# Optimization experiments

Hardware: AMD Instinct MI355X
Metric: run time of the kernel (lower is better)

The kernel has to match this reference:

```python
import jax, jax.numpy as jnp
import numpy as np
import math

N = 100000   # nodes
E = 500000   # edges
IN_C = 128
EDGE_D = 64
HEADS = 4
OUT_C = 32
HC = HEADS * OUT_C  # 128


def setup_inputs() -> dict:
    key = jax.random.key(0)
    ks = jax.random.split(key, 12)
    s_in = 1.0 / math.sqrt(IN_C)
    s_e = 1.0 / math.sqrt(EDGE_D)
    return {
        "x": jax.random.normal(ks[0], (N, IN_C), jnp.float32),
        "edge_index": jax.random.randint(ks[1], (2, E), 0, N, dtype=jnp.int32),
        "edge_attr": jax.random.normal(ks[2], (E, EDGE_D), jnp.float32),
        "Wq": jax.random.uniform(ks[3], (HC, IN_C), jnp.float32, -s_in, s_in),
        "bq": jax.random.uniform(ks[4], (HC,), jnp.float32, -s_in, s_in),
        "Wk": jax.random.uniform(ks[5], (HC, IN_C), jnp.float32, -s_in, s_in),
        "bk": jax.random.uniform(ks[6], (HC,), jnp.float32, -s_in, s_in),
        "Wv": jax.random.uniform(ks[7], (HC, IN_C), jnp.float32, -s_in, s_in),
        "bv": jax.random.uniform(ks[8], (HC,), jnp.float32, -s_in, s_in),
        "We": jax.random.uniform(ks[9], (HC, EDGE_D), jnp.float32, -s_e, s_e),
        "Ws": jax.random.uniform(ks[10], (HC, IN_C), jnp.float32, -s_in, s_in),
        "bs": jax.random.uniform(ks[11], (HC,), jnp.float32, -s_in, s_in),
    }


def reference(x, edge_index, edge_attr, Wq, bq, Wk, bk, Wv, bv, We, Ws, bs):
    src = edge_index[0]
    dst = edge_index[1]
    x_i = x[dst]                       # [E, IN_C] target-node feats
    x_j = x[src]                       # [E, IN_C] source-node feats

    e = (edge_attr @ We.T).reshape(E, HEADS, OUT_C)
    q = (x_i @ Wq.T + bq).reshape(E, HEADS, OUT_C)
    k = (x_j @ Wk.T + bk).reshape(E, HEADS, OUT_C) + e

    alpha = jnp.sum(q * k, axis=-1) / jnp.sqrt(jnp.float32(OUT_C))  # [E, H]
    # Faithful to the source: GLOBAL per-column max (not per-segment), then
    # segment-sum of exponentials over destination nodes.
    m = jnp.max(alpha, axis=0)                                      # [H]
    exp_a = jnp.exp(alpha - m)                                      # [E, H]
    denom = jax.ops.segment_sum(exp_a, dst, num_segments=N)         # [N, H]
    alpha = exp_a / (denom[dst] + 1e-16)                            # [E, H]

    v = (x_j @ Wv.T + bv).reshape(E, HEADS, OUT_C) + e
    msg = v * alpha[:, :, None]                                     # [E, H, C]

    out = jax.ops.segment_sum(msg.reshape(E, HC), dst, num_segments=N)  # [N, HC]
    out = out + (x @ Ws.T + bs)
    return out
```

## Files before the change

kernel.cpp:

```cpp
#include <hip/hip_runtime.h>
#include <hip/hip_bf16.h>
#include <math.h>

#define N_NODES 100000
#define N_EDGES 500000
#define M0 8.0f
#define INV_SQRT32 0.17677669529663687f

#define NB_HIST 1954
#define NB_PROJ 1563
#define NB_EE   3907
#define GRID_MEGA (NB_HIST + NB_PROJ + NB_EE)

typedef __attribute__((ext_vector_type(8))) short bf16x8;
typedef __attribute__((ext_vector_type(4))) float f32x4;
typedef __attribute__((ext_vector_type(8))) unsigned short us8;

static __device__ __forceinline__ unsigned short f2bf(float f) {
    __hip_bfloat16 h = __float2bfloat16(f);
    return *(unsigned short*)&h;
}

static __device__ __forceinline__ void split4(float4 v, ushort4& hv, ushort4& lv) {
    const unsigned short h0 = f2bf(v.x), h1 = f2bf(v.y),
                         h2 = f2bf(v.z), h3 = f2bf(v.w);
    hv.x = h0; hv.y = h1; hv.z = h2; hv.w = h3;
    lv.x = f2bf(v.x - __uint_as_float((unsigned)h0 << 16));
    lv.y = f2bf(v.y - __uint_as_float((unsigned)h1 << 16));
    lv.z = f2bf(v.z - __uint_as_float((unsigned)h2 << 16));
    lv.w = f2bf(v.w - __uint_as_float((unsigned)h3 << 16));
}

__global__ __launch_bounds__(256) void prep_kernel(
    const float* __restrict__ Wq, const float* __restrict__ Wk,
    const float* __restrict__ Wv, const float* __restrict__ Ws,
    const float* __restrict__ We,
    unsigned short* __restrict__ WBh, unsigned short* __restrict__ WBl,
    unsigned short* __restrict__ WEh, unsigned short* __restrict__ WEl,
    int* __restrict__ cursor)
{
    const int i = blockIdx.x * 256 + threadIdx.x;
    if (i < N_NODES) cursor[i] = 0;
    if (i < 65536) {
        const int p = i >> 14;
        const float* W = (p == 0) ? Wq : (p == 1) ? Wk : (p == 2) ? Wv : Ws;
        const float v = W[i & 16383];
        const unsigned short h = f2bf(v);
        WBh[i] = h;
        WBl[i] = f2bf(v - __uint_as_float((unsigned)h << 16));
    } else if (i < 73728) {
        const int idx = i - 65536;
        const float v = We[idx];
        const unsigned short h = f2bf(v);
        WEh[idx] = h;
        WEl[idx] = f2bf(v - __uint_as_float((unsigned)h << 16));
    }
}

__global__ __launch_bounds__(256) void mega_kernel(
    const float* __restrict__ x, const int* __restrict__ ei,
    const float* __restrict__ ea,
    const unsigned short* __restrict__ WBh, const unsigned short* __restrict__ WBl,
    const unsigned short* __restrict__ WEh, const unsigned short* __restrict__ WEl,
    const float* __restrict__ bq, const float* __restrict__ bk,
    const float* __restrict__ bv, const float* __restrict__ bs,
    float* __restrict__ Qn, float* __restrict__ Kn, float* __restrict__ Vn,
    float* __restrict__ out, unsigned short* __restrict__ Ee,
    int* __restrict__ cursor)
{
    __shared__ __align__(16) unsigned short sAh[8192];
    __shared__ __align__(16) unsigned short sAl[8192];
    __shared__ __align__(16) unsigned short sWh[8192];
    __shared__ __align__(16) unsigned short sWl[8192];

    const int t = threadIdx.x;
    const int bid = blockIdx.x;

    if (bid < NB_HIST) {
        const int e = bid * 256 + t;
        if (e < N_EDGES) atomicAdd(&cursor[ei[N_EDGES + e]], 1);
        return;
    }

    const int lane = t & 63;
    const int fr = lane & 15;
    const int fq = lane >> 4;

    if (bid < NB_HIST + NB_PROJ) {
        const long r0 = (long)(bid - NB_HIST) * 64;
        const int wid = t >> 6;

        for (int i = t; i < 2048; i += 256) {
            const int r = i >> 5;
            const int k4 = (i & 31) * 4;
            const long row = r0 + r;
            float4 v = (row < N_NODES) ? *(const float4*)&x[row * 128 + k4]
                                       : make_float4(0.f, 0.f, 0.f, 0.f);
            ushort4 hv, lv; split4(v, hv, lv);
            const int di = r * 128 + (k4 ^ ((r & 7) << 3));
            *(ushort4*)&sAh[di] = hv;
            *(ushort4*)&sAl[di] = lv;
        }

        for (int p = 0; p < 4; ++p) {
            const float* bias = (p == 0) ? bq : (p == 1) ? bk : (p == 2) ? bv : bs;
            float* dst        = (p == 0) ? Qn : (p == 1) ? Kn : (p == 2) ? Vn : out;

            f32x4 acc[4][2];
#pragma unroll
            for (int m = 0; m < 4; ++m)
#pragma unroll
                for (int n = 0; n < 2; ++n) acc[m][n] = (f32x4){0.f, 0.f, 0.f, 0.f};

            for (int kc = 0; kc < 2; ++kc) {
                __syncthreads();
                for (int i = t; i < 1024; i += 256) {
                    const int r = i >> 3;
                    const int s = i & 7;
                    const int gi = p * 16384 + r * 128 + kc * 64 + s * 8;
                    const int di = r * 64 + ((s * 8) ^ ((r & 7) << 3));
                    *(us8*)&sWh[di] = *(const us8*)&WBh[gi];
                    *(us8*)&sWl[di] = *(const us8*)&WBl[gi];
                }
                __syncthreads();

#pragma unroll
                for (int ks = 0; ks < 2; ++ks) {
                    const int kx = kc * 64 + ks * 32 + fq * 8;
                    const int kw = ks * 32 + fq * 8;
                    bf16x8 ah[4], al[4], bh[2], bl[2];
#pragma unroll
                    for (int m = 0; m < 4; ++m) {
                        const int r = m * 16 + fr;
                        const int di = r * 128 + (kx ^ ((r & 7) << 3));
                        ah[m] = *(const bf16x8*)&sAh[di];
                        al[m] = *(const bf16x8*)&sAl[di];
                    }
#pragma unroll
                    for (int n = 0; n < 2; ++n) {
                        const int r = wid * 32 + n * 16 + fr;
                        const int di = r * 64 + (kw ^ ((r & 7) << 3));
                        bh[n] = *(const bf16x8*)&sWh[di];
                        bl[n] = *(const bf16x8*)&sWl[di];
                    }
#pragma unroll
                    for (int m = 0; m < 4; ++m)
#pragma unroll
                        for (int n = 0; n < 2; ++n) {
                            acc[m][n] = __builtin_amdgcn_mfma_f32_16x16x32_bf16(
                                ah[m], bh[n], acc[m][n], 0, 0, 0);
                            acc[m][n] = __builtin_amdgcn_mfma_f32_16x16x32_bf16(
                                ah[m], bl[n], acc[m][n], 0, 0, 0);
                            acc[m][n] = __builtin_amdgcn_mfma_f32_16x16x32_bf16(
                                al[m], bh[n], acc[m][n], 0, 0, 0);
                        }
                }
            }

            float bb[2];
#pragma unroll
            for (int n = 0; n < 2; ++n) bb[n] = bias[wid * 32 + n * 16 + fr];
#pragma unroll
            for (int m = 0; m < 4; ++m) {
                const long rowb = r0 + m * 16 + fq * 4;
#pragma unroll
                for (int j = 0; j < 4; ++j) {
                    if (rowb + j < N_NODES) {
#pragma unroll
                        for (int n = 0; n < 2; ++n)
                            dst[(rowb + j) * 128 + wid * 32 + n * 16 + fr] =
                                acc[m][n][j] + bb[n];
                    }
                }
            }
        }
    } else {
        const long e0 = (long)(bid - NB_HIST - NB_PROJ) * 128;
        const int wr = (t >> 6) >> 1;
        const int wc = (t >> 6) & 1;

        for (int i = t; i < 1024; i += 256) {
            const int r = i >> 3;
            const int s = i & 7;
            const int di = r * 64 + ((s * 8) ^ ((r & 7) << 3));
            *(us8*)&sWh[di] = *(const us8*)&WEh[r * 64 + s * 8];
            *(us8*)&sWl[di] = *(const us8*)&WEl[r * 64 + s * 8];
        }
        for (int i = t; i < 2048; i += 256) {
            const int r = i >> 4;
            const int k4 = (i & 15) * 4;
            const long e = e0 + r;
            float4 v = (e < N_EDGES) ? *(const float4*)&ea[e * 64 + k4]
                                     : make_float4(0.f, 0.f, 0.f, 0.f);
            ushort4 hv, lv; split4(v, hv, lv);
            const int di = r * 64 + (k4 ^ ((r & 7) << 3));
            *(ushort4*)&sAh[di] = hv;
            *(ushort4*)&sAl[di] = lv;
        }
        __syncthreads();

        f32x4 acc[4][4];
#pragma unroll
        for (int m = 0; m < 4; ++m)
#pragma unroll
            for (int n = 0; n < 4; ++n) acc[m][n] = (f32x4){0.f, 0.f, 0.f, 0.f};

#pragma unroll
        for (int ks = 0; ks < 2; ++ks) {
            const int kk = ks * 32 + fq * 8;
            bf16x8 ah[4], al[4], bh[4], bl[4];
#pragma unroll
            for (int m = 0; m < 4; ++m) {
                const int r = wr * 64 + m * 16 + fr;
                const int di = r * 64 + (kk ^ ((r & 7) << 3));
                ah[m] = *(const bf16x8*)&sAh[di];
                al[m] = *(const bf16x8*)&sAl[di];
            }
#pragma unroll
            for (int n = 0; n < 4; ++n) {
                const int r = wc * 64 + n * 16 + fr;
                const int di = r * 64 + (kk ^ ((r & 7) << 3));
                bh[n] = *(const bf16x8*)&sWh[di];
                bl[n] = *(const bf16x8*)&sWl[di];
            }
#pragma unroll
            for (int m = 0; m < 4; ++m)
#pragma unroll
                for (int n = 0; n < 4; ++n) {
                    acc[m][n] = __builtin_amdgcn_mfma_f32_16x16x32_bf16(
                        ah[m], bh[n], acc[m][n], 0, 0, 0);
                    acc[m][n] = __builtin_amdgcn_mfma_f32_16x16x32_bf16(
                        ah[m], bl[n], acc[m][n], 0, 0, 0);
                    acc[m][n] = __builtin_amdgcn_mfma_f32_16x16x32_bf16(
                        al[m], bh[n], acc[m][n], 0, 0, 0);
                }
        }

#pragma unroll
        for (int m = 0; m < 4; ++m) {
            const long erow = e0 + wr * 64 + m * 16 + fq * 4;
#pragma unroll
            for (int j = 0; j < 4; ++j) {
                if (erow + j < N_EDGES) {
#pragma unroll
                    for (int n = 0; n < 4; ++n)
                        Ee[(erow + j) * 128 + wc * 64 + n * 16 + fr] =
                            f2bf(acc[m][n][j]);
                }
            }
        }
    }
}

__global__ __launch_bounds__(1024) void csr_scan_kernel(
    int* __restrict__ cursor, int* __restrict__ csr_off)
{
    __shared__ int wsum[16];
    const int t = threadIdx.x;
    const int lane = t & 63;
    const int wid = t >> 6;
    const int n0 = t * 100;
    const bool active = (t < 1000);

    int tsum = 0;
    if (active) {
        for (int q = 0; q < 25; ++q) {
            const int4 d = *(const int4*)&cursor[n0 + q * 4];
            tsum += d.x + d.y + d.z + d.w;
        }
    }
    int inc = tsum;
#pragma unroll
    for (int o = 1; o < 64; o <<= 1) {
        const int v = __shfl_up(inc, o, 64);
        if (lane >= o) inc += v;
    }
    if (lane == 63) wsum[wid] = inc;
    __syncthreads();
    if (t == 0) {
        int run = 0;
#pragma unroll
        for (int w = 0; w < 16; ++w) { const int v = wsum[w]; wsum[w] = run; run += v; }
        csr_off[N_NODES] = run;
    }
    __syncthreads();
    if (active) {
        int run = wsum[wid] + inc - tsum;
        for (int q = 0; q < 25; ++q) {
            const int n = n0 + q * 4;
            const int4 d = *(const int4*)&cursor[n];
            int4 offv;
            offv.x = run; run += d.x;
            offv.y = run; run += d.y;
            offv.z = run; run += d.z;
            offv.w = run; run += d.w;
            *(int4*)&csr_off[n] = offv;
            *(int4*)&cursor[n]  = offv;
        }
    }
}

__global__ __launch_bounds__(256) void csr_fill_kernel(
    const int* __restrict__ ei, int* __restrict__ cursor,
    int* __restrict__ csr_eid, int* __restrict__ csr_src)
{
    const int e = blockIdx.x * 256 + threadIdx.x;
    if (e >= N_EDGES) return;
    const int dst = ei[N_EDGES + e];
    const int pos = atomicAdd(&cursor[dst], 1);
    csr_eid[pos] = e;
    csr_src[pos] = ei[e];
}

__global__ __launch_bounds__(256) void fused_attn_kernel(
    const int* __restrict__ csr_off, const int* __restrict__ csr_eid,
    const int* __restrict__ csr_src, const unsigned short* __restrict__ Ee,
    const float* __restrict__ Qn, const float* __restrict__ Kn,
    const float* __restrict__ Vn, float* __restrict__ out)
{
    const int lane = threadIdx.x & 63;
    const int l2 = lane * 2;
    const long n = (long)blockIdx.x * 4 + (threadIdx.x >> 6);

    const int off0 = csr_off[n];
    const int off1 = csr_off[n + 1];
    const float2 q = *(const float2*)&Qn[n * 128 + l2];

    float dsum = 0.f;
    float2 acc = make_float2(0.f, 0.f);
    for (int base = off0; base < off1; base += 64) {
        const int cnt = min(64, off1 - base);
        int eid = 0, src = 0;
        if (base + lane < off1) {
            eid = csr_eid[base + lane];
            src = csr_src[base + lane];
        }
        for (int j = 0; j < cnt; ++j) {
            const long e = __shfl(eid, j, 64);
            const long s = __shfl(src, j, 64);
            const unsigned u = *(const unsigned*)&Ee[e * 128 + l2];
            const float2 k = *(const float2*)&Kn[s * 128 + l2];
            const float ea0 = __uint_as_float(u << 16);
            const float ea1 = __uint_as_float(u & 0xffff0000u);
            float p = q.x * (k.x + ea0) + q.y * (k.y + ea1);
#pragma unroll
            for (int o = 1; o < 16; o <<= 1) p += __shfl_xor(p, o, 64);
            const float an = __expf(p * INV_SQRT32 - M0);
            dsum += an;
            const float2 v = *(const float2*)&Vn[s * 128 + l2];
            acc.x = fmaf(v.x + ea0, an, acc.x);
            acc.y = fmaf(v.y + ea1, an, acc.y);
        }
    }
    const float rd = 1.f / (dsum + 1e-16f);
    float2 o = *(const float2*)&out[n * 128 + l2];
    o.x = fmaf(acc.x, rd, o.x);
    o.y = fmaf(acc.y, rd, o.y);
    *(float2*)&out[n * 128 + l2] = o;
}

extern "C" void kernel_launch(void* const* d_in, const int* in_sizes, int n_in,
                              void* d_out, int out_size, void* d_ws, size_t ws_size,
                              hipStream_t stream)
{
    const float* x  = (const float*)d_in[0];
    const int*   ei = (const int*)d_in[1];
    const float* ea = (const float*)d_in[2];
    const float* Wq = (const float*)d_in[3];
    const float* bq = (const float*)d_in[4];
    const float* Wk = (const float*)d_in[5];
    const float* bk = (const float*)d_in[6];
    const float* Wv = (const float*)d_in[7];
    const float* bv = (const float*)d_in[8];
    const float* We = (const float*)d_in[9];
    const float* Ws = (const float*)d_in[10];
    const float* bs = (const float*)d_in[11];
    float* out = (float*)d_out;

    float* ws = (float*)d_ws;
    float* Qn = ws;
    float* Kn = ws + 12800000;
    float* Vn = ws + 25600000;
    int* csr_off = (int*)(ws + 38400000);
    int* cursor  = (int*)(ws + 38500004);
    int* csr_eid = (int*)(ws + 38600004);
    int* csr_src = (int*)(ws + 39100004);
    unsigned short* WBh = (unsigned short*)(ws + 40000000);
    unsigned short* WBl = (unsigned short*)(ws + 40050000);
    unsigned short* WEh = (unsigned short*)(ws + 40100000);
    unsigned short* WEl = (unsigned short*)(ws + 40110000);
    unsigned short* Ee = (unsigned short*)((char*)d_ws + 163200032);

    prep_kernel<<<391, 256, 0, stream>>>(Wq, Wk, Wv, Ws, We,
                                         WBh, WBl, WEh, WEl, cursor);

    mega_kernel<<<GRID_MEGA, 256, 0, stream>>>(x, ei, ea,
                                               WBh, WBl, WEh, WEl,
                                               bq, bk, bv, bs,
                                               Qn, Kn, Vn, out, Ee, cursor);

    csr_scan_kernel<<<1, 1024, 0, stream>>>(cursor, csr_off);

    csr_fill_kernel<<<NB_HIST, 256, 0, stream>>>(ei, cursor, csr_eid, csr_src);

    fused_attn_kernel<<<25000, 256, 0, stream>>>(csr_off, csr_eid, csr_src, Ee,
                                                 Qn, Kn, Vn, out);
}
```

Baseline: 599.6 us.

## Use 512-thread mega blocks, direct global-to-LDS loads, merged histogram and packed CSR

Doubles the mega kernel's block size to 512 threads, splitting each projection and edge-embedding tile across more waves so each wave holds fewer accumulators. Weight tiles now go straight into LDS through global_load_lds, with the swizzle moved to the global address. The edge-histogram atomics are folded into the edge-embedding blocks instead of running in separate blocks. CSR edge id and source are packed into one int2 array so the attention kernel does a single load per edge. The changes aim to cut register pressure, staging instructions and launch work, but less reuse per wave may cost MFMA efficiency.

```diff
diff --git a/kernel.cpp b/kernel.cpp
--- a/kernel.cpp
+++ b/kernel.cpp
@@ -7,10 +7,9 @@
 #define M0 8.0f
 #define INV_SQRT32 0.17677669529663687f
 
-#define NB_HIST 1954
 #define NB_PROJ 1563
 #define NB_EE   3907
-#define GRID_MEGA (NB_HIST + NB_PROJ + NB_EE)
+#define GRID_MEGA (NB_PROJ + NB_EE)
 
 typedef __attribute__((ext_vector_type(8))) short bf16x8;
 typedef __attribute__((ext_vector_type(4))) float f32x4;
@@ -29,6 +28,14 @@
     lv.y = f2bf(v.y - __uint_as_float((unsigned)h1 << 16));
     lv.z = f2bf(v.z - __uint_as_float((unsigned)h2 << 16));
     lv.w = f2bf(v.w - __uint_as_float((unsigned)h3 << 16));
+}
+
+static __device__ __forceinline__ void gl_lds16(
+    const unsigned short* __restrict__ g, unsigned short* l)
+{
+    __builtin_amdgcn_global_load_lds(
+        (const __attribute__((address_space(1))) unsigned int*)g,
+        (__attribute__((address_space(3))) unsigned int*)l, 16, 0, 0);
 }
 
 __global__ __launch_bounds__(256) void prep_kernel(
@@ -57,7 +64,7 @@
     }
 }
 
-__global__ __launch_bounds__(256) void mega_kernel(
+__global__ __launch_bounds__(512, 4) void mega_kernel(
     const float* __restrict__ x, const int* __restrict__ ei,
     const float* __restrict__ ea,
     const unsigned short* __restrict__ WBh, const unsigned short* __restrict__ WBl,
@@ -76,21 +83,15 @@
     const int t = threadIdx.x;
     const int bid = blockIdx.x;
 
-    if (bid < NB_HIST) {
-        const int e = bid * 256 + t;
-        if (e < N_EDGES) atomicAdd(&cursor[ei[N_EDGES + e]], 1);
-        return;
-    }
-
     const int lane = t & 63;
+    const int wid = t >> 6;
     const int fr = lane & 15;
     const int fq = lane >> 4;
 
-    if (bid < NB_HIST + NB_PROJ) {
-        const long r0 = (long)(bid - NB_HIST) * 64;
-        const int wid = t >> 6;
-
-        for (int i = t; i < 2048; i += 256) {
+    if (bid < NB_PROJ) {
+        const long r0 = (long)bid * 64;
+
+        for (int i = t; i < 2048; i += 512) {
             const int r = i >> 5;
             const int k4 = (i & 31) * 4;
             const long row = r0 + r;
@@ -106,21 +107,20 @@
             const float* bias = (p == 0) ? bq : (p == 1) ? bk : (p == 2) ? bv : bs;
             float* dst        = (p == 0) ? Qn : (p == 1) ? Kn : (p == 2) ? Vn : out;
 
-            f32x4 acc[4][2];
-#pragma unroll
-            for (int m = 0; m < 4; ++m)
-#pragma unroll
-                for (int n = 0; n < 2; ++n) acc[m][n] = (f32x4){0.f, 0.f, 0.f, 0.f};
+            f32x4 acc[4];
+#pragma unroll
+            for (int m = 0; m < 4; ++m) acc[m] = (f32x4){0.f, 0.f, 0.f, 0.f};
 
             for (int kc = 0; kc < 2; ++kc) {
                 __syncthreads();
-                for (int i = t; i < 1024; i += 256) {
+#pragma unroll
+                for (int c = 0; c < 2; ++c) {
+                    const int i = c * 512 + t;
                     const int r = i >> 3;
-                    const int s = i & 7;
-                    const int gi = p * 16384 + r * 128 + kc * 64 + s * 8;
-                    const int di = r * 64 + ((s * 8) ^ ((r & 7) << 3));
-                    *(us8*)&sWh[di] = *(const us8*)&WBh[gi];
-                    *(us8*)&sWl[di] = *(const us8*)&WBl[gi];
+                    const int d = i & 7;
+                    const int gi = p * 16384 + r * 128 + kc * 64 + ((d ^ (r & 7)) * 8);
+                    gl_lds16(&WBh[gi], &sWh[i * 8]);
+                    gl_lds16(&WBl[gi], &sWl[i * 8]);
                 }
                 __syncthreads();
 
@@ -128,7 +128,7 @@
                 for (int ks = 0; ks < 2; ++ks) {
                     const int kx = kc * 64 + ks * 32 + fq * 8;
                     const int kw = ks * 32 + fq * 8;
-                    bf16x8 ah[4], al[4], bh[2], bl[2];
+                    bf16x8 ah[4], al[4], wh, wl;
 #pragma unroll
                     for (int m = 0; m < 4; ++m) {
                         const int r = m * 16 + fr;
@@ -136,57 +136,55 @@
                         ah[m] = *(const bf16x8*)&sAh[di];
                         al[m] = *(const bf16x8*)&sAl[di];
                     }
-#pragma unroll
-                    for (int n = 0; n < 2; ++n) {
-                        const int r = wid * 32 + n * 16 + fr;
+                    {
+                        const int r = wid * 16 + fr;
                         const int di = r * 64 + (kw ^ ((r & 7) << 3));
-                        bh[n] = *(const bf16x8*)&sWh[di];
-                        bl[n] = *(const bf16x8*)&sWl[di];
+                        wh = *(const bf16x8*)&sWh[di];
+                        wl = *(const bf16x8*)&sWl[di];
                     }
 #pragma unroll
-                    for (int m = 0; m < 4; ++m)
-#pragma unroll
-                        for (int n = 0; n < 2; ++n) {
-                            acc[m][n] = __builtin_amdgcn_mfma_f32_16x16x32_bf16(
-                                ah[m], bh[n], acc[m][n], 0, 0, 0);
-                            acc[m][n] = __builtin_amdgcn_mfma_f32_16x16x32_bf16(
-                                ah[m], bl[n], acc[m][n], 0, 0, 0);
-                            acc[m][n] = __builtin_amdgcn_mfma_f32_16x16x32_bf16(
-                                al[m], bh[n], acc[m][n], 0, 0, 0);
-                        }
-                }
-            }
-
-            float bb[2];
-#pragma unroll
-            for (int n = 0; n < 2; ++n) bb[n] = bias[wid * 32 + n * 16 + fr];
-#pragma unroll
-            for (int m = 0; m < 4; ++m) {
-                const long rowb = r0 + m * 16 + fq * 4;
-#pragma unroll
-                for (int j = 0; j < 4; ++j) {
-                    if (rowb + j < N_NODES) {
-#pragma unroll
-                        for (int n = 0; n < 2; ++n)
-                            dst[(rowb + j) * 128 + wid * 32 + n * 16 + fr] =
-                                acc[m][n][j] + bb[n];
+                    for (int m = 0; m < 4; ++m) {
+                        acc[m] = __builtin_amdgcn_mfma_f32_16x16x32_bf16(
+                            ah[m], wh, acc[m], 0, 0, 0);
+                        acc[m] = __builtin_amdgcn_mfma_f32_16x16x32_bf16(
+                            ah[m], wl, acc[m], 0, 0, 0);
+                        acc[m] = __builtin_amdgcn_mfma_f32_16x16x32_bf16(
+                            al[m], wh, acc[m], 0, 0, 0);
                     }
                 }
             }
+
+            const float bb = bias[wid * 16 + fr];
+#pragma unroll
+            for (int m = 0; m < 4; ++m) {
+                const long rowb = r0 + m * 16 + fq * 4;
+#pragma unroll
+                for (int j = 0; j < 4; ++j) {
+                    if (rowb + j < N_NODES)
+                        dst[(rowb + j) * 128 + wid * 16 + fr] = acc[m][j] + bb;
+                }
+            }
         }
     } else {
-        const long e0 = (long)(bid - NB_HIST - NB_PROJ) * 128;
-        const int wr = (t >> 6) >> 1;
-        const int wc = (t >> 6) & 1;
-
-        for (int i = t; i < 1024; i += 256) {
+        const long e0 = (long)(bid - NB_PROJ) * 128;
+        const int wr = wid >> 2;
+        const int wc = wid & 3;
+
+        if (t < 128) {
+            const long e = e0 + t;
+            if (e < N_EDGES) atomicAdd(&cursor[ei[N_EDGES + e]], 1);
+        }
+
+#pragma unroll
+        for (int c = 0; c < 2; ++c) {
+            const int i = c * 512 + t;
             const int r = i >> 3;
-            const int s = i & 7;
-            const int di = r * 64 + ((s * 8) ^ ((r & 7) << 3));
-            *(us8*)&sWh[di] = *(const us8*)&WEh[r * 64 + s * 8];
-            *(us8*)&sWl[di] = *(const us8*)&WEl[r * 64 + s * 8];
-        }
-        for (int i = t; i < 2048; i += 256) {
+            const int d = i & 7;
+            const int gi = r * 64 + ((d ^ (r & 7)) * 8);
+            gl_lds16(&WEh[gi], &sWh[i * 8]);
+            gl_lds16(&WEl[gi], &sWl[i * 8]);
+        }
+        for (int i = t; i < 2048; i += 512) {
             const int r = i >> 4;
             const int k4 = (i & 15) * 4;
             const long e = e0 + r;
@@ -199,16 +197,16 @@
         }
         __syncthreads();
 
-        f32x4 acc[4][4];
+        f32x4 acc[4][2];
 #pragma unroll
         for (int m = 0; m < 4; ++m)
 #pragma unroll
-            for (int n = 0; n < 4; ++n) acc[m][n] = (f32x4){0.f, 0.f, 0.f, 0.f};
+            for (int n = 0; n < 2; ++n) acc[m][n] = (f32x4){0.f, 0.f, 0.f, 0.f};
 
 #pragma unroll
         for (int ks = 0; ks < 2; ++ks) {
             const int kk = ks * 32 + fq * 8;
-            bf16x8 ah[4], al[4], bh[4], bl[4];
+            bf16x8 ah[4], al[4], wh[2], wl[2];
 #pragma unroll
             for (int m = 0; m < 4; ++m) {
                 const int r = wr * 64 + m * 16 + fr;
@@ -217,34 +215,34 @@
                 al[m] = *(const bf16x8*)&sAl[di];
             }
 #pragma unroll
-            for (int n = 0; n < 4; ++n) {
-                const int r = wc * 64 + n * 16 + fr;
+            for (int n = 0; n < 2; ++n) {
+                const int r = wc * 32 + n * 16 + fr;
                 const int di = r * 64 + (kk ^ ((r & 7) << 3));
-                bh[n] = *(const bf16x8*)&sWh[di];
-                bl[n] = *(const bf16x8*)&sWl[di];
+                wh[n] = *(const bf16x8*)&sWh[di];
+                wl[n] = *(const bf16x8*)&sWl[di];
             }
 #pragma unroll
             for (int m = 0; m < 4; ++m)
 #pragma unroll
-                for (int n = 0; n < 4; ++n) {
+                for (int n = 0; n < 2; ++n) {
                     acc[m][n] = __builtin_amdgcn_mfma_f32_16x16x32_bf16(
-                        ah[m], bh[n], acc[m][n], 0, 0, 0);
+                        ah[m], wh[n], acc[m][n], 0, 0, 0);
                     acc[m][n] = __builtin_amdgcn_mfma_f32_16x16x32_bf16(
-                        ah[m], bl[n], acc[m][n], 0, 0, 0);
+                        ah[m], wl[n], acc[m][n], 0, 0, 0);
                     acc[m][n] = __builtin_amdgcn_mfma_f32_16x16x32_bf16(
-                        al[m], bh[n], acc[m][n], 0, 0, 0);
+                        al[m], wh[n], acc[m][n], 0, 0, 0);
                 }
         }
 
 #pragma unroll
         for (int m = 0; m < 4; ++m) {
-            const long erow = e0 + wr * 64 + m * 16 + fq * 4;
+            const long e = e0 + wr * 64 + m * 16 + fq * 4;
 #pragma unroll
             for (int j = 0; j < 4; ++j) {
-                if (erow + j < N_EDGES) {
-#pragma unroll
-                    for (int n = 0; n < 4; ++n)
-                        Ee[(erow + j) * 128 + wc * 64 + n * 16 + fr] =
+                if (e + j < N_EDGES) {
+#pragma unroll
+                    for (int n = 0; n < 2; ++n)
+                        Ee[(e + j) * 128 + wc * 32 + n * 16 + fr] =
                             f2bf(acc[m][n][j]);
                 }
             }
@@ -302,19 +300,18 @@
 
 __global__ __launch_bounds__(256) void csr_fill_kernel(
     const int* __restrict__ ei, int* __restrict__ cursor,
-    int* __restrict__ csr_eid, int* __restrict__ csr_src)
+    int2* __restrict__ csr_es)
 {
     const int e = blockIdx.x * 256 + threadIdx.x;
     if (e >= N_EDGES) return;
     const int dst = ei[N_EDGES + e];
     const int pos = atomicAdd(&cursor[dst], 1);
-    csr_eid[pos] = e;
-    csr_src[pos] = ei[e];
+    csr_es[pos] = make_int2(e, ei[e]);
 }
 
 __global__ __launch_bounds__(256) void fused_attn_kernel(
-    const int* __restrict__ csr_off, const int* __restrict__ csr_eid,
-    const int* __restrict__ csr_src, const unsigned short* __restrict__ Ee,
+    const int* __restrict__ csr_off, const int2* __restrict__ csr_es,
+    const unsigned short* __restrict__ Ee,
     const float* __restrict__ Qn, const float* __restrict__ Kn,
     const float* __restrict__ Vn, float* __restrict__ out)
 {
@@ -330,14 +327,11 @@
     float2 acc = make_float2(0.f, 0.f);
     for (int base = off0; base < off1; base += 64) {
         const int cnt = min(64, off1 - base);
-        int eid = 0, src = 0;
-        if (base + lane < off1) {
-            eid = csr_eid[base + lane];
-            src = csr_src[base + lane];
-        }
+        int2 es = make_int2(0, 0);
+        if (base + lane < off1) es = csr_es[base + lane];
         for (int j = 0; j < cnt; ++j) {
-            const long e = __shfl(eid, j, 64);
-            const long s = __shfl(src, j, 64);
+            const long e = __shfl(es.x, j, 64);
+            const long s = __shfl(es.y, j, 64);
             const unsigned u = *(const unsigned*)&Ee[e * 128 + l2];
             const float2 k = *(const float2*)&Kn[s * 128 + l2];
             const float ea0 = __uint_as_float(u << 16);
@@ -383,8 +377,7 @@
     float* Vn = ws + 25600000;
     int* csr_off = (int*)(ws + 38400000);
     int* cursor  = (int*)(ws + 38500004);
-    int* csr_eid = (int*)(ws + 38600004);
-    int* csr_src = (int*)(ws + 39100004);
+    int2* csr_es = (int2*)(ws + 38600004);
     unsigned short* WBh = (unsigned short*)(ws + 40000000);
     unsigned short* WBl = (unsigned short*)(ws + 40050000);
     unsigned short* WEh = (unsigned short*)(ws + 40100000);
@@ -394,15 +387,15 @@
     prep_kernel<<<391, 256, 0, stream>>>(Wq, Wk, Wv, Ws, We,
                                          WBh, WBl, WEh, WEl, cursor);
 
-    mega_kernel<<<GRID_MEGA, 256, 0, stream>>>(x, ei, ea,
+    mega_kernel<<<GRID_MEGA, 512, 0, stream>>>(x, ei, ea,
                                                WBh, WBl, WEh, WEl,
                                                bq, bk, bv, bs,
                                                Qn, Kn, Vn, out, Ee, cursor);
 
     csr_scan_kernel<<<1, 1024, 0, stream>>>(cursor, csr_off);
 
-    csr_fill_kernel<<<NB_HIST, 256, 0, stream>>>(ei, cursor, csr_eid, csr_src);
-
-    fused_attn_kernel<<<25000, 256, 0, stream>>>(csr_off, csr_eid, csr_src, Ee,
+    csr_fill_kernel<<<(N_EDGES + 255) / 256, 256, 0, stream>>>(ei, cursor, csr_es);
+
+    fused_attn_kernel<<<25000, 256, 0, stream>>>(csr_off, csr_es, Ee,
                                                  Qn, Kn, Vn, out);
 }
```

Measured after the change: 551.4 us. 1.09x faster.
